# Performance work log

Hardware: AMD Instinct MI355X
Metric: run time of the kernel (lower is better)

Reference implementation:

```python
import jax, jax.numpy as jnp
import numpy as np

EPS = 1e-5

def rmsnorm(x, w):
    var = jnp.mean(x * x, axis=-1, keepdims=True)
    return x * jax.lax.rsqrt(var + EPS) * w

def apply_rope(x, cos, sin):
    # x: [B, S, H, D], cos/sin: [S, D//2]; llama-style complex rotation over pairs
    B, S, H, D = x.shape
    xr = x.reshape(B, S, H, D // 2, 2)
    x0, x1 = xr[..., 0], xr[..., 1]
    c = cos[None, :, None, :]
    s = sin[None, :, None, :]
    o0 = x0 * c - x1 * s
    o1 = x0 * s + x1 * c
    return jnp.stack([o0, o1], axis=-1).reshape(B, S, H, D)

def setup_inputs() -> dict:
    key = jax.random.key(0)
    ks = jax.random.split(key, 8)
    B, S, dim = 2, 2048, 2048
    H, nope, rope = 16, 128, 64
    q_lr, kv_lr = 1536, 512
    hd = nope + rope
    x = jax.random.normal(ks[0], (B, S, dim), jnp.float32)
    wd_q = jax.random.normal(ks[1], (dim, q_lr), jnp.float32) * (dim ** -0.5)
    wu_q = jax.random.normal(ks[2], (q_lr, H * hd), jnp.float32) * (q_lr ** -0.5)
    q_norm_w = jnp.ones((q_lr,), jnp.float32)
    wd_kv = jax.random.normal(ks[3], (dim, kv_lr + rope), jnp.float32) * (dim ** -0.5)
    wu_kv = jax.random.normal(ks[4], (kv_lr, H * 2 * nope), jnp.float32) * (kv_lr ** -0.5)
    kv_norm_w = jnp.ones((kv_lr,), jnp.float32)
    wo = jax.random.normal(ks[5], (H * nope, dim), jnp.float32) * ((H * nope) ** -0.5)
    pos = jnp.arange(S, dtype=jnp.float32)
    inv_freq = 1.0 / (10000.0 ** (jnp.arange(0, rope, 2, dtype=jnp.float32) / rope))
    ang = pos[:, None] * inv_freq[None, :]  # [S, rope//2]
    return {"x": x, "wd_q": wd_q, "wu_q": wu_q, "q_norm_w": q_norm_w,
            "wd_kv": wd_kv, "wu_kv": wu_kv, "kv_norm_w": kv_norm_w, "wo": wo,
            "cos": jnp.cos(ang), "sin": jnp.sin(ang), "start_pos": 0}

def reference(x, wd_q, wu_q, q_norm_w, wd_kv, wu_kv, kv_norm_w, wo, cos, sin, start_pos):
    B, S, dim = x.shape
    H, nope, rope = 16, 128, 64
    kv_lr = 512
    hd = nope + rope
    # low-rank Q projection + RMSNorm
    cq = x @ wd_q
    xq = rmsnorm(cq, q_norm_w) @ wu_q
    xq = xq.reshape(B, S, H, hd)
    xq_nope, xq_rope = xq[..., :nope], xq[..., nope:]
    # low-rank KV projection
    kvd = x @ wd_kv
    ckv, xk_rope = kvd[..., :kv_lr], kvd[..., kv_lr:]
    xk_rope = xk_rope.reshape(B, S, 1, rope)
    kvu = (rmsnorm(ckv, kv_norm_w) @ wu_kv).reshape(B, S, H, 2 * nope)
    xk_nope, xv = kvu[..., :nope], kvu[..., nope:]
    # partial RoPE
    xq_rope = apply_rope(xq_rope, cos, sin)
    xk_rope = apply_rope(xk_rope, cos, sin)
    xk_rope = jnp.broadcast_to(xk_rope, (B, S, H, rope))
    q = jnp.concatenate([xq_nope, xq_rope], axis=-1)  # [B,S,H,192]
    k = jnp.concatenate([xk_nope, xk_rope], axis=-1)
    # causal SDPA
    scale = 1.0 / jnp.sqrt(jnp.float32(hd))
    scores = jnp.einsum('bqhd,bkhd->bhqk', q, k) * scale
    mask = jnp.tril(jnp.ones((S, S), bool))
    scores = jnp.where(mask[None, None], scores, jnp.finfo(scores.dtype).min)
    attn = jax.nn.softmax(scores, axis=-1)
    out = jnp.einsum('bhqk,bkhd->bqhd', attn, xv).reshape(B, S, H * nope)
    return out @ wo
```

## Files before the change

kernel.cpp:

```cpp
#include <hip/hip_runtime.h>
#include <hip/hip_bf16.h>

#define S_LEN 2048
#define NHEAD 16
#define NOPE 128
#define ROPE 64
#define HD 192

typedef unsigned short ushort_t;
typedef __attribute__((ext_vector_type(8))) short short8;
typedef __attribute__((ext_vector_type(4))) float f32x4;

#define AS1 __attribute__((address_space(1)))
#define AS3 __attribute__((address_space(3)))

__device__ __forceinline__ unsigned short f2bf(float f) {
  unsigned int u = __float_as_uint(f);
  return (unsigned short)((u + 0x7FFFu + ((u >> 16) & 1u)) >> 16);
}

__global__ __launch_bounds__(256) void cast_f32_bf16_k(const float* __restrict__ in,
                                                       ushort_t* __restrict__ out) {
  const int i = blockIdx.x * 256 + threadIdx.x;
  const float4 v0 = *(const float4*)&in[(size_t)i * 8];
  const float4 v1 = *(const float4*)&in[(size_t)i * 8 + 4];
  union { uint4 u; ushort_t s[8]; } pk;
  pk.s[0] = f2bf(v0.x); pk.s[1] = f2bf(v0.y); pk.s[2] = f2bf(v0.z); pk.s[3] = f2bf(v0.w);
  pk.s[4] = f2bf(v1.x); pk.s[5] = f2bf(v1.y); pk.s[6] = f2bf(v1.z); pk.s[7] = f2bf(v1.w);
  *(uint4*)&out[(size_t)i * 8] = pk.u;
}

__global__ __launch_bounds__(256) void transpose_cast_k(const float* __restrict__ B,
                                                        ushort_t* __restrict__ Bt,
                                                        int K, int N) {
  __shared__ float tile[32][33];
  const int tx = threadIdx.x & 31, ty = threadIdx.x >> 5;
  const int n0 = blockIdx.x * 32, k0 = blockIdx.y * 32;
  if (n0 >= N) {
#pragma unroll
    for (int r = 0; r < 4; ++r)
      Bt[(size_t)(n0 + ty + 8 * r) * K + k0 + tx] = 0;
    return;
  }
#pragma unroll
  for (int r = 0; r < 4; ++r)
    tile[ty + 8 * r][tx] = B[(size_t)(k0 + ty + 8 * r) * N + n0 + tx];
  __syncthreads();
#pragma unroll
  for (int r = 0; r < 4; ++r)
    Bt[(size_t)(n0 + ty + 8 * r) * K + k0 + tx] = f2bf(tile[tx][ty + 8 * r]);
}

template<int EPI>
__global__ __launch_bounds__(256) void mfma_gemm(const ushort_t* __restrict__ A,
                                                 const ushort_t* __restrict__ Bt,
                                                 float* __restrict__ C,
                                                 int M, int N, int K, int ldc,
                                                 ushort_t* __restrict__ kb16o,
                                                 ushort_t* __restrict__ vto,
                                                 float* __restrict__ C2) {
  __shared__ ushort_t As[128 * 32];
  __shared__ ushort_t Bs[128 * 32];
  const int tid = threadIdx.x;
  const int lane = tid & 63;
  const int wave = tid >> 6;
  const int wm = wave & 1, wn = wave >> 1;

  unsigned bxu = blockIdx.x, byu = blockIdx.y;
  {
    const unsigned gx = gridDim.x;
    const unsigned nwg = gx * gridDim.y;
    if ((nwg & 7u) == 0u) {
      unsigned flat = byu * gx + bxu;
      const unsigned cpx = nwg >> 3;
      flat = (flat & 7u) * cpx + (flat >> 3);
      bxu = flat % gx; byu = flat / gx;
    }
  }
  const int m0 = byu * 128, n0 = bxu * 128;
  const int l15 = lane & 15, quad = lane >> 4;

  f32x4 acc[4][4] = {};

  const int it0 = tid, it1 = tid + 256;
  const int ma0 = it0 >> 2, kc0 = it0 & 3;
  const int ma1 = it1 >> 2, kc1 = it1 & 3;

  typedef AS3 ushort_t lds_us;
  lds_us* AsL = (lds_us*)As;
  lds_us* BsL = (lds_us*)Bs;
  const int wbase = wave * 512;

  for (int k0 = 0; k0 < K; k0 += 32) {
    __builtin_amdgcn_global_load_lds(
        (const AS1 void*)&A[(size_t)(m0 + ma0) * K + k0 + kc0 * 8],
        (AS3 void*)(AsL + wbase), 16, 0, 0);
    __builtin_amdgcn_global_load_lds(
        (const AS1 void*)&A[(size_t)(m0 + ma1) * K + k0 + kc1 * 8],
        (AS3 void*)(AsL + 2048 + wbase), 16, 0, 0);
    __builtin_amdgcn_global_load_lds(
        (const AS1 void*)&Bt[(size_t)(n0 + ma0) * K + k0 + kc0 * 8],
        (AS3 void*)(BsL + wbase), 16, 0, 0);
    __builtin_amdgcn_global_load_lds(
        (const AS1 void*)&Bt[(size_t)(n0 + ma1) * K + k0 + kc1 * 8],
        (AS3 void*)(BsL + 2048 + wbase), 16, 0, 0);
    __syncthreads();

    short8 af[4], bf[4];
#pragma unroll
    for (int i = 0; i < 4; ++i)
      af[i] = *(const short8*)&As[(wm * 64 + i * 16 + l15) * 32 + quad * 8];
#pragma unroll
    for (int j = 0; j < 4; ++j)
      bf[j] = *(const short8*)&Bs[(wn * 64 + j * 16 + l15) * 32 + quad * 8];
#pragma unroll
    for (int i = 0; i < 4; ++i)
#pragma unroll
      for (int j = 0; j < 4; ++j)
        acc[i][j] = __builtin_amdgcn_mfma_f32_16x16x32_bf16(af[i], bf[j], acc[i][j], 0, 0, 0);
    __syncthreads();
  }

  if constexpr (EPI == 0) {
#pragma unroll
    for (int i = 0; i < 4; ++i)
#pragma unroll
      for (int r = 0; r < 4; ++r) {
        const size_t rg = (size_t)(m0 + wm * 64 + i * 16 + quad * 4 + r);
#pragma unroll
        for (int j = 0; j < 4; ++j)
          C[rg * ldc + n0 + wn * 64 + j * 16 + l15] = acc[i][j][r];
      }
  } else if constexpr (EPI == 1) {
    const int h = n0 >> 8;
    const bool is_v = (n0 >> 7) & 1;
    if (!is_v) {
#pragma unroll
      for (int i = 0; i < 4; ++i)
#pragma unroll
        for (int r = 0; r < 4; ++r) {
          const size_t rg = (size_t)(m0 + wm * 64 + i * 16 + quad * 4 + r);
#pragma unroll
          for (int j = 0; j < 4; ++j)
            kb16o[rg * 2048 + h * 128 + wn * 64 + j * 16 + l15] = f2bf(acc[i][j][r]);
        }
    } else {
      __shared__ __align__(16) ushort_t trb[64 * 136];
      const int bb = m0 >> 11;
      const int m0loc = m0 & 2047;
      ushort_t* vbase = vto + ((size_t)(bb * NHEAD + h) * 128) * 2048;
#pragma unroll
      for (int vh = 0; vh < 2; ++vh) {
        if (wn == vh) {
#pragma unroll
          for (int i = 0; i < 4; ++i)
#pragma unroll
            for (int r = 0; r < 4; ++r) {
              const int tloc = wm * 64 + i * 16 + quad * 4 + r;
#pragma unroll
              for (int j = 0; j < 4; ++j)
                trb[(j * 16 + l15) * 136 + tloc] = f2bf(acc[i][j][r]);
            }
        }
        __syncthreads();
#pragma unroll
        for (int it = 0; it < 4; ++it) {
          const int u = tid + (it << 8);
          const int vdl = u >> 4, tc = u & 15;
          *(uint4*)&vbase[(size_t)(vh * 64 + vdl) * 2048 + m0loc + tc * 8] =
              *(const uint4*)&trb[vdl * 136 + tc * 8];
        }
        __syncthreads();
      }
    }
  } else {
    float* Cd;
    int ldd, nc;
    if (n0 < 1536) { Cd = C;  ldd = 1536; nc = n0; }
    else           { Cd = C2; ldd = 640;  nc = n0 - 1536; }
#pragma unroll
    for (int i = 0; i < 4; ++i)
#pragma unroll
      for (int r = 0; r < 4; ++r) {
        const size_t rg = (size_t)(m0 + wm * 64 + i * 16 + quad * 4 + r);
#pragma unroll
        for (int j = 0; j < 4; ++j)
          Cd[rg * ldd + nc + wn * 64 + j * 16 + l15] = acc[i][j][r];
      }
  }
}

__global__ __launch_bounds__(256) void rmsnorm2_k(const float* __restrict__ cq,
                                                  ushort_t* __restrict__ cqn,
                                                  const float* __restrict__ qw,
                                                  const float* __restrict__ kvd,
                                                  ushort_t* __restrict__ ckvn,
                                                  const float* __restrict__ kvw) {
  const bool is_q = blockIdx.x < 4096;
  const int row = blockIdx.x & 4095;
  const int tid = threadIdx.x;
  const float* ip = is_q ? cq + (size_t)row * 1536 : kvd + (size_t)row * 640;
  ushort_t* op = is_q ? cqn + (size_t)row * 1536 : ckvn + (size_t)row * 512;
  const float* w = is_q ? qw : kvw;
  const int L = is_q ? 1536 : 512;
  const int nper = L >> 8;
  float r[6];
  float ss = 0.f;
  for (int j = 0; j < nper; ++j) {
    r[j] = ip[tid + (j << 8)];
    ss += r[j] * r[j];
  }
  for (int off = 32; off; off >>= 1) ss += __shfl_down(ss, off);
  __shared__ float wsum[4];
  __shared__ float scale_s;
  if ((tid & 63) == 0) wsum[tid >> 6] = ss;
  __syncthreads();
  if (tid == 0) {
    float t = wsum[0] + wsum[1] + wsum[2] + wsum[3];
    scale_s = rsqrtf(t / (float)L + 1e-5f);
  }
  __syncthreads();
  const float sc = scale_s;
  for (int j = 0; j < nper; ++j)
    op[tid + (j << 8)] = f2bf(r[j] * sc * w[tid + (j << 8)]);
}

__global__ __launch_bounds__(512) void rope_k(float* __restrict__ qall,
                                              const float* __restrict__ kvd,
                                              ushort_t* __restrict__ krope16,
                                              const float* __restrict__ cosb,
                                              const float* __restrict__ sinb) {
  const int row = blockIdx.x;
  const int s = row & (S_LEN - 1);
  const int tid = threadIdx.x;
  const int d = tid & 31, h = tid >> 5;
  const float c = cosb[s * 32 + d];
  const float sn = sinb[s * 32 + d];
  float* qb = qall + (size_t)row * 3072 + h * HD + NOPE;
  float x0 = qb[2 * d], x1 = qb[2 * d + 1];
  qb[2 * d]     = x0 * c - x1 * sn;
  qb[2 * d + 1] = x0 * sn + x1 * c;
  if (tid < 32) {
    const float* kb = kvd + (size_t)row * 640 + 512;
    float y0 = kb[2 * d], y1 = kb[2 * d + 1];
    union { unsigned int u; ushort_t s2[2]; } pk;
    pk.s2[0] = f2bf(y0 * c - y1 * sn);
    pk.s2[1] = f2bf(y0 * sn + y1 * c);
    *(unsigned int*)&krope16[(size_t)row * 64 + 2 * d] = pk.u;
  }
}

#define QT 128
#define KC 64
__global__ __launch_bounds__(256, 2) void attn_k(const float* __restrict__ qall,
                                                 const ushort_t* __restrict__ kb16,
                                                 const ushort_t* __restrict__ vT,
                                                 const ushort_t* __restrict__ krope16,
                                                 ushort_t* __restrict__ outp) {
  const int bx = blockIdx.x;
  const int second = bx >> 8;
  const int h = (bx >> 4) & 15;
  int tile = bx & 15;
  if (second) tile = 15 - tile;
  const int b = second;
  const int q0 = tile * QT;
  const int tid = threadIdx.x;
  const int lane = tid & 63;
  const int wq = tid >> 6;
  const int l15 = lane & 15, quad = lane >> 4;

  __shared__ __align__(16) ushort_t Kn[64 * 128];
  __shared__ __align__(16) ushort_t Kr[64 * 64];
  __shared__ __align__(16) ushort_t Vt[2][128 * 64];
  __shared__ __align__(16) ushort_t Pb[4][32 * 72];

  const int qbase = q0 + wq * 32;
  const size_t growq = (size_t)b * S_LEN + qbase;
  const ushort_t* vTh = vT + ((size_t)(b * NHEAD + h) * 128) * 2048;
  const size_t bbase = (size_t)b * S_LEN;

  typedef AS3 ushort_t lds_us;
  lds_us* KnL = (lds_us*)Kn;
  lds_us* KrL = (lds_us*)Kr;
  lds_us* VtL = (lds_us*)Vt;
  const int wbase = wq * 512;

  auto issueK = [&](int c) {
    const size_t growk = bbase + (size_t)c * KC;
#pragma unroll
    for (int it = 0; it < 4; ++it) {
      const int u = tid + (it << 8);
      const int key = u >> 4, s = u & 15;
      const int ss = s ^ (key & 7);
      __builtin_amdgcn_global_load_lds(
          (const AS1 void*)&kb16[(growk + key) * 2048 + h * 128 + ss * 8],
          (AS3 void*)(KnL + wbase + it * 2048), 16, 0, 0);
    }
#pragma unroll
    for (int it = 0; it < 2; ++it) {
      const int u = tid + (it << 8);
      const int key = u >> 3, s = u & 7;
      const int ss = s ^ (key & 7);
      __builtin_amdgcn_global_load_lds(
          (const AS1 void*)&krope16[(growk + key) * 64 + ss * 8],
          (AS3 void*)(KrL + wbase + it * 2048), 16, 0, 0);
    }
  };
  auto issueV = [&](int c, int buf) {
    const int j0 = c * KC;
#pragma unroll
    for (int it = 0; it < 4; ++it) {
      const int u = tid + (it << 8);
      const int vd = u >> 3, s = u & 7;
      const int ss = s ^ (vd & 7);
      __builtin_amdgcn_global_load_lds(
          (const AS1 void*)&vTh[(size_t)vd * 2048 + j0 + ss * 8],
          (AS3 void*)(VtL + buf * 8192 + wbase + it * 2048), 16, 0, 0);
    }
  };

  issueK(0);
  issueV(0, 0);
  __builtin_amdgcn_sched_barrier(0);

  const float scale = 0.07216878364870323f;
  short8 qf[2][6];
#pragma unroll
  for (int mt = 0; mt < 2; ++mt)
#pragma unroll
    for (int ks = 0; ks < 6; ++ks) {
      const float* src = &qall[(growq + mt * 16 + l15) * 3072 + h * HD + ks * 32 + quad * 8];
      const float4 v0 = *(const float4*)src;
      const float4 v1 = *(const float4*)(src + 4);
      union { short8 s8; ushort_t u[8]; } pk;
      pk.u[0] = f2bf(v0.x * scale); pk.u[1] = f2bf(v0.y * scale);
      pk.u[2] = f2bf(v0.z * scale); pk.u[3] = f2bf(v0.w * scale);
      pk.u[4] = f2bf(v1.x * scale); pk.u[5] = f2bf(v1.y * scale);
      pk.u[6] = f2bf(v1.z * scale); pk.u[7] = f2bf(v1.w * scale);
      qf[mt][ks] = pk.s8;
    }

  f32x4 oacc[2][8] = {};
  float mrow[2][4], lrow[2][4];
  int q_r[2][4];
#pragma unroll
  for (int mt = 0; mt < 2; ++mt)
#pragma unroll
    for (int r = 0; r < 4; ++r) {
      mrow[mt][r] = -1e30f; lrow[mt][r] = 0.f;
      q_r[mt][r] = qbase + mt * 16 + quad * 4 + r;
    }

  const int nchunk = (q0 + QT) / KC;

  asm volatile("s_waitcnt vmcnt(4)" ::: "memory");
  __builtin_amdgcn_s_barrier();
  __builtin_amdgcn_sched_barrier(0);

  for (int c = 0; c < nchunk; ++c) {
    const int j0 = c * KC;
    const bool more = (c + 1 < nchunk);
    const int buf = c & 1;
    const bool skipw = (j0 > qbase + 31);

    f32x4 sacc[2][4] = {};
    if (!skipw) {
      __builtin_amdgcn_s_setprio(1);
#pragma unroll
      for (int ks = 0; ks < 6; ++ks) {
        short8 kf[4];
        if (ks < 4) {
#pragma unroll
          for (int kt = 0; kt < 4; ++kt)
            kf[kt] = *(const short8*)&Kn[(kt * 16 + l15) * 128 + (((ks * 4 + quad) ^ (l15 & 7)) << 3)];
        } else {
#pragma unroll
          for (int kt = 0; kt < 4; ++kt)
            kf[kt] = *(const short8*)&Kr[(kt * 16 + l15) * 64 + ((((ks - 4) * 4 + quad) ^ (l15 & 7)) << 3)];
        }
#pragma unroll
        for (int mt = 0; mt < 2; ++mt)
#pragma unroll
          for (int kt = 0; kt < 4; ++kt)
            sacc[mt][kt] = __builtin_amdgcn_mfma_f32_16x16x32_bf16(qf[mt][ks], kf[kt], sacc[mt][kt], 0, 0, 0);
      }
      __builtin_amdgcn_s_setprio(0);
    }

    __builtin_amdgcn_s_barrier();
    if (more) issueK(c + 1);
    __builtin_amdgcn_sched_barrier(0);

    if (!skipw) {
      if (j0 + KC - 1 > qbase) {
#pragma unroll
        for (int mt = 0; mt < 2; ++mt)
#pragma unroll
          for (int kt = 0; kt < 4; ++kt) {
            const int key = j0 + kt * 16 + l15;
#pragma unroll
            for (int r = 0; r < 4; ++r)
              sacc[mt][kt][r] = (key <= q_r[mt][r]) ? sacc[mt][kt][r] : -1e30f;
          }
      }
      float pmax[2][4];
#pragma unroll
      for (int mt = 0; mt < 2; ++mt)
#pragma unroll
        for (int r = 0; r < 4; ++r) {
          float mx = fmaxf(fmaxf(sacc[mt][0][r], sacc[mt][1][r]),
                           fmaxf(sacc[mt][2][r], sacc[mt][3][r]));
          mx = fmaxf(mx, __shfl_xor(mx, 1));
          mx = fmaxf(mx, __shfl_xor(mx, 2));
          mx = fmaxf(mx, __shfl_xor(mx, 4));
          mx = fmaxf(mx, __shfl_xor(mx, 8));
          pmax[mt][r] = mx;
        }
      bool need = false;
#pragma unroll
      for (int mt = 0; mt < 2; ++mt)
#pragma unroll
        for (int r = 0; r < 4; ++r)
          need = need || (pmax[mt][r] > mrow[mt][r] + 8.0f);
      const bool upd = __any(need);
      float alpha[2][4];
      if (upd) {
#pragma unroll
        for (int mt = 0; mt < 2; ++mt)
#pragma unroll
          for (int r = 0; r < 4; ++r) {
            const float mn = fmaxf(mrow[mt][r], pmax[mt][r]);
            alpha[mt][r] = __expf(mrow[mt][r] - mn);
            mrow[mt][r] = mn;
          }
      }
#pragma unroll
      for (int mt = 0; mt < 2; ++mt)
#pragma unroll
        for (int kt = 0; kt < 4; ++kt)
#pragma unroll
          for (int r = 0; r < 4; ++r)
            sacc[mt][kt][r] = __expf(sacc[mt][kt][r] - mrow[mt][r]);
#pragma unroll
      for (int mt = 0; mt < 2; ++mt)
#pragma unroll
        for (int r = 0; r < 4; ++r) {
          float rs = sacc[mt][0][r] + sacc[mt][1][r] + sacc[mt][2][r] + sacc[mt][3][r];
          rs += __shfl_xor(rs, 1);
          rs += __shfl_xor(rs, 2);
          rs += __shfl_xor(rs, 4);
          rs += __shfl_xor(rs, 8);
          lrow[mt][r] = upd ? lrow[mt][r] * alpha[mt][r] + rs : lrow[mt][r] + rs;
        }
#pragma unroll
      for (int mt = 0; mt < 2; ++mt)
#pragma unroll
        for (int kt = 0; kt < 4; ++kt)
#pragma unroll
          for (int r = 0; r < 4; ++r)
            Pb[wq][(mt * 16 + quad * 4 + r) * 72 + kt * 16 + l15] = f2bf(sacc[mt][kt][r]);
      if (upd) {
#pragma unroll
        for (int mt = 0; mt < 2; ++mt)
#pragma unroll
          for (int nt = 0; nt < 8; ++nt)
#pragma unroll
            for (int r = 0; r < 4; ++r)
              oacc[mt][nt][r] *= alpha[mt][r];
      }
    }

    if (more) asm volatile("s_waitcnt vmcnt(6)" ::: "memory");
    else      asm volatile("s_waitcnt vmcnt(0)" ::: "memory");
    __builtin_amdgcn_s_barrier();
    __builtin_amdgcn_sched_barrier(0);

    if (!skipw) {
      __builtin_amdgcn_s_setprio(1);
#pragma unroll
      for (int st = 0; st < 2; ++st) {
        short8 pf[2];
#pragma unroll
        for (int mt = 0; mt < 2; ++mt)
          pf[mt] = *(const short8*)&Pb[wq][(mt * 16 + l15) * 72 + st * 32 + quad * 8];
#pragma unroll
        for (int nt = 0; nt < 8; ++nt) {
          const short8 vf = *(const short8*)&Vt[buf][(nt * 16 + l15) * 64 + (((st * 4 + quad) ^ (l15 & 7)) << 3)];
#pragma unroll
          for (int mt = 0; mt < 2; ++mt)
            oacc[mt][nt] = __builtin_amdgcn_mfma_f32_16x16x32_bf16(pf[mt], vf, oacc[mt][nt], 0, 0, 0);
        }
      }
      __builtin_amdgcn_s_setprio(0);
    }

    if (more) {
      issueV(c + 1, buf ^ 1);
      __builtin_amdgcn_sched_barrier(0);
      asm volatile("s_waitcnt vmcnt(4)" ::: "memory");
      __builtin_amdgcn_s_barrier();
      __builtin_amdgcn_sched_barrier(0);
    }
  }

#pragma unroll
  for (int mt = 0; mt < 2; ++mt)
#pragma unroll
    for (int r = 0; r < 4; ++r) {
      const float inv = 1.0f / lrow[mt][r];
      const size_t orow = growq + mt * 16 + quad * 4 + r;
#pragma unroll
      for (int nt = 0; nt < 8; ++nt)
        outp[orow * 2048 + h * 128 + nt * 16 + l15] = f2bf(oacc[mt][nt][r] * inv);
    }
}

extern "C" void kernel_launch(void* const* d_in, const int* in_sizes, int n_in,
                              void* d_out, int out_size, void* d_ws, size_t ws_size,
                              hipStream_t stream) {
  const float* x        = (const float*)d_in[0];
  const float* wd_q     = (const float*)d_in[1];
  const float* wu_q     = (const float*)d_in[2];
  const float* q_norm_w = (const float*)d_in[3];
  const float* wd_kv    = (const float*)d_in[4];
  const float* wu_kv    = (const float*)d_in[5];
  const float* kv_norm_w= (const float*)d_in[6];
  const float* wo       = (const float*)d_in[7];
  const float* cosb     = (const float*)d_in[8];
  const float* sinb     = (const float*)d_in[9];
  float* out = (float*)d_out;

  char* ws = (char*)d_ws;
  float*    qall  = (float*)(ws + 0);
  float*    cq    = (float*)(ws + 0);
  ushort_t* kb16  = (ushort_t*)(ws + 50331648);
  ushort_t* vT    = (ushort_t*)(ws + 67108864);
  ushort_t* xb    = (ushort_t*)(ws + 83886080);
  ushort_t* cqn   = (ushort_t*)(ws + 117440512);
  float*    kvd   = (float*)(ws + 130023424);
  ushort_t* ckvn  = (ushort_t*)(ws + 140509184);
  ushort_t* aoutb = (ushort_t*)(ws + 130023424);
  ushort_t* krope16 = (ushort_t*)(ws + 146800640);
  ushort_t* wdqt  = (ushort_t*)(ws + 147849216);
  ushort_t* wdkvt = (ushort_t*)(ws + 154140672);
  ushort_t* wuqt  = (ushort_t*)(ws + 156762112);
  ushort_t* wukvt = (ushort_t*)(ws + 166199296);
  ushort_t* wot   = (ushort_t*)(ws + 170393600);

  const int M = 2 * S_LEN;
  dim3 blk(256);

  cast_f32_bf16_k<<<4096, blk, 0, stream>>>(x, xb);

  transpose_cast_k<<<dim3(1536 / 32, 2048 / 32), blk, 0, stream>>>(wd_q, wdqt, 2048, 1536);
  transpose_cast_k<<<dim3(640 / 32, 2048 / 32), blk, 0, stream>>>(wd_kv, wdkvt, 2048, 576);
  transpose_cast_k<<<dim3(3072 / 32, 1536 / 32), blk, 0, stream>>>(wu_q, wuqt, 1536, 3072);
  transpose_cast_k<<<dim3(4096 / 32, 512 / 32), blk, 0, stream>>>(wu_kv, wukvt, 512, 4096);
  transpose_cast_k<<<dim3(2048 / 32, 2048 / 32), blk, 0, stream>>>(wo, wot, 2048, 2048);

  mfma_gemm<2><<<dim3(2176 / 128, M / 128), blk, 0, stream>>>(
      xb, wdqt, cq, M, 2176, 2048, 1536, nullptr, nullptr, kvd);
  rmsnorm2_k<<<2 * M, 256, 0, stream>>>(cq, cqn, q_norm_w, kvd, ckvn, kv_norm_w);
  mfma_gemm<0><<<dim3(3072 / 128, M / 128), blk, 0, stream>>>(
      cqn, wuqt, qall, M, 3072, 1536, 3072, nullptr, nullptr, nullptr);
  mfma_gemm<1><<<dim3(4096 / 128, M / 128), blk, 0, stream>>>(
      ckvn, wukvt, nullptr, M, 4096, 512, 0, kb16, vT, nullptr);
  rope_k<<<M, 512, 0, stream>>>(qall, kvd, krope16, cosb, sinb);
  attn_k<<<2 * NHEAD * (S_LEN / QT), 256, 0, stream>>>(qall, kb16, vT, krope16, aoutb);
  mfma_gemm<0><<<dim3(2048 / 128, M / 128), blk, 0, stream>>>(
      aoutb, wot, out, M, 2048, 2048, 2048, nullptr, nullptr, nullptr);
}
```

Baseline: 511.7 us.

## Fuse Q RoPE/scale/bf16 into Q-up GEMM epilogue, merge prep kernels, reorder attention grid

Merges the x cast and five weight transpose-casts into one prep kernel, cutting launch count. The Q up-projection GEMM gets a new epilogue that applies the softmax scale and RoPE (via lane-pair shuffles) and writes bf16 directly. This removes the fp32 Q round trip and the separate Q RoPE pass, and attention now loads bf16 Q fragments directly. The attention block-index mapping is changed to interleave heads and batches with a causal tile pairing for load balance, and the K-rope kernel shrinks to K only.

Result: faster. 496.5 us (-3.0%).

```diff
diff --git a/kernel.cpp b/kernel.cpp
--- a/kernel.cpp
+++ b/kernel.cpp
@@ -19,23 +19,33 @@
   return (unsigned short)((u + 0x7FFFu + ((u >> 16) & 1u)) >> 16);
 }
 
-__global__ __launch_bounds__(256) void cast_f32_bf16_k(const float* __restrict__ in,
-                                                       ushort_t* __restrict__ out) {
-  const int i = blockIdx.x * 256 + threadIdx.x;
-  const float4 v0 = *(const float4*)&in[(size_t)i * 8];
-  const float4 v1 = *(const float4*)&in[(size_t)i * 8 + 4];
-  union { uint4 u; ushort_t s[8]; } pk;
-  pk.s[0] = f2bf(v0.x); pk.s[1] = f2bf(v0.y); pk.s[2] = f2bf(v0.z); pk.s[3] = f2bf(v0.w);
-  pk.s[4] = f2bf(v1.x); pk.s[5] = f2bf(v1.y); pk.s[6] = f2bf(v1.z); pk.s[7] = f2bf(v1.w);
-  *(uint4*)&out[(size_t)i * 8] = pk.u;
-}
-
-__global__ __launch_bounds__(256) void transpose_cast_k(const float* __restrict__ B,
-                                                        ushort_t* __restrict__ Bt,
-                                                        int K, int N) {
+__global__ __launch_bounds__(256) void prep_k(const float* __restrict__ x, ushort_t* __restrict__ xb,
+                                              const float* __restrict__ wd_q, ushort_t* __restrict__ wdqt,
+                                              const float* __restrict__ wd_kv, ushort_t* __restrict__ wdkvt,
+                                              const float* __restrict__ wu_q, ushort_t* __restrict__ wuqt,
+                                              const float* __restrict__ wu_kv, ushort_t* __restrict__ wukvt,
+                                              const float* __restrict__ wo, ushort_t* __restrict__ wot) {
+  int id = blockIdx.x;
+  if (id < 4096) {
+    const int i = id * 256 + threadIdx.x;
+    const float4 v0 = *(const float4*)&x[(size_t)i * 8];
+    const float4 v1 = *(const float4*)&x[(size_t)i * 8 + 4];
+    union { uint4 u; ushort_t s[8]; } pk;
+    pk.s[0] = f2bf(v0.x); pk.s[1] = f2bf(v0.y); pk.s[2] = f2bf(v0.z); pk.s[3] = f2bf(v0.w);
+    pk.s[4] = f2bf(v1.x); pk.s[5] = f2bf(v1.y); pk.s[6] = f2bf(v1.z); pk.s[7] = f2bf(v1.w);
+    *(uint4*)&xb[(size_t)i * 8] = pk.u;
+    return;
+  }
+  id -= 4096;
+  const float* B; ushort_t* Bt; int K, N, gx;
+  if (id < 3072)               { B = wd_q;  Bt = wdqt;  K = 2048; N = 1536; gx = 48;  }
+  else if ((id -= 3072) < 1280){ B = wd_kv; Bt = wdkvt; K = 2048; N = 576;  gx = 20;  }
+  else if ((id -= 1280) < 4608){ B = wu_q;  Bt = wuqt;  K = 1536; N = 3072; gx = 96;  }
+  else if ((id -= 4608) < 2048){ B = wu_kv; Bt = wukvt; K = 512;  N = 4096; gx = 128; }
+  else { id -= 2048;             B = wo;    Bt = wot;   K = 2048; N = 2048; gx = 64;  }
   __shared__ float tile[32][33];
   const int tx = threadIdx.x & 31, ty = threadIdx.x >> 5;
-  const int n0 = blockIdx.x * 32, k0 = blockIdx.y * 32;
+  const int n0 = (id % gx) * 32, k0 = (id / gx) * 32;
   if (n0 >= N) {
 #pragma unroll
     for (int r = 0; r < 4; ++r)
@@ -58,7 +68,9 @@
                                                  int M, int N, int K, int ldc,
                                                  ushort_t* __restrict__ kb16o,
                                                  ushort_t* __restrict__ vto,
-                                                 float* __restrict__ C2) {
+                                                 float* __restrict__ C2,
+                                                 const float* __restrict__ cosb,
+                                                 const float* __restrict__ sinb) {
   __shared__ ushort_t As[128 * 32];
   __shared__ ushort_t Bs[128 * 32];
   const int tid = threadIdx.x;
@@ -173,7 +185,7 @@
         __syncthreads();
       }
     }
-  } else {
+  } else if constexpr (EPI == 2) {
     float* Cd;
     int ldd, nc;
     if (n0 < 1536) { Cd = C;  ldd = 1536; nc = n0; }
@@ -186,6 +198,30 @@
 #pragma unroll
         for (int j = 0; j < 4; ++j)
           Cd[rg * ldd + nc + wn * 64 + j * 16 + l15] = acc[i][j][r];
+      }
+  } else {
+    const float qscale = 0.07216878364870323f;
+#pragma unroll
+    for (int i = 0; i < 4; ++i)
+#pragma unroll
+      for (int r = 0; r < 4; ++r) {
+        const int rg = m0 + wm * 64 + i * 16 + quad * 4 + r;
+        const int sp = rg & (S_LEN - 1);
+#pragma unroll
+        for (int j = 0; j < 4; ++j) {
+          const int col = n0 + wn * 64 + j * 16 + l15;
+          float val = acc[i][j][r] * qscale;
+          const float pr = __shfl_xor(val, 1);
+          const int dd = col % HD;
+          float o = val;
+          if (dd >= NOPE) {
+            const int d = (dd - NOPE) >> 1;
+            const float cc = cosb[sp * 32 + d];
+            const float sn = sinb[sp * 32 + d];
+            o = (lane & 1) ? (pr * sn + val * cc) : (val * cc - pr * sn);
+          }
+          kb16o[(size_t)rg * 3072 + col] = f2bf(o);
+        }
       }
   }
 }
@@ -225,44 +261,36 @@
     op[tid + (j << 8)] = f2bf(r[j] * sc * w[tid + (j << 8)]);
 }
 
-__global__ __launch_bounds__(512) void rope_k(float* __restrict__ qall,
-                                              const float* __restrict__ kvd,
-                                              ushort_t* __restrict__ krope16,
-                                              const float* __restrict__ cosb,
-                                              const float* __restrict__ sinb) {
-  const int row = blockIdx.x;
+__global__ __launch_bounds__(256) void rope_kr_k(const float* __restrict__ kvd,
+                                                 ushort_t* __restrict__ krope16,
+                                                 const float* __restrict__ cosb,
+                                                 const float* __restrict__ sinb) {
+  const int tid = threadIdx.x;
+  const int row = blockIdx.x * 8 + (tid >> 5);
+  const int d = tid & 31;
   const int s = row & (S_LEN - 1);
-  const int tid = threadIdx.x;
-  const int d = tid & 31, h = tid >> 5;
   const float c = cosb[s * 32 + d];
   const float sn = sinb[s * 32 + d];
-  float* qb = qall + (size_t)row * 3072 + h * HD + NOPE;
-  float x0 = qb[2 * d], x1 = qb[2 * d + 1];
-  qb[2 * d]     = x0 * c - x1 * sn;
-  qb[2 * d + 1] = x0 * sn + x1 * c;
-  if (tid < 32) {
-    const float* kb = kvd + (size_t)row * 640 + 512;
-    float y0 = kb[2 * d], y1 = kb[2 * d + 1];
-    union { unsigned int u; ushort_t s2[2]; } pk;
-    pk.s2[0] = f2bf(y0 * c - y1 * sn);
-    pk.s2[1] = f2bf(y0 * sn + y1 * c);
-    *(unsigned int*)&krope16[(size_t)row * 64 + 2 * d] = pk.u;
-  }
+  const float* kb = kvd + (size_t)row * 640 + 512;
+  const float y0 = kb[2 * d], y1 = kb[2 * d + 1];
+  union { unsigned int u; ushort_t s2[2]; } pk;
+  pk.s2[0] = f2bf(y0 * c - y1 * sn);
+  pk.s2[1] = f2bf(y0 * sn + y1 * c);
+  *(unsigned int*)&krope16[(size_t)row * 64 + 2 * d] = pk.u;
 }
 
 #define QT 128
 #define KC 64
-__global__ __launch_bounds__(256, 2) void attn_k(const float* __restrict__ qall,
+__global__ __launch_bounds__(256, 2) void attn_k(const ushort_t* __restrict__ q16,
                                                  const ushort_t* __restrict__ kb16,
                                                  const ushort_t* __restrict__ vT,
                                                  const ushort_t* __restrict__ krope16,
                                                  ushort_t* __restrict__ outp) {
   const int bx = blockIdx.x;
-  const int second = bx >> 8;
-  const int h = (bx >> 4) & 15;
-  int tile = bx & 15;
-  if (second) tile = 15 - tile;
-  const int b = second;
+  const int g = bx & 31;
+  const int s = bx >> 5;
+  const int tile = (s < 8) ? s : 23 - s;
+  const int b = g >> 4, h = g & 15;
   const int q0 = tile * QT;
   const int tid = threadIdx.x;
   const int lane = tid & 63;
@@ -290,8 +318,8 @@
 #pragma unroll
     for (int it = 0; it < 4; ++it) {
       const int u = tid + (it << 8);
-      const int key = u >> 4, s = u & 15;
-      const int ss = s ^ (key & 7);
+      const int key = u >> 4, sl = u & 15;
+      const int ss = sl ^ (key & 7);
       __builtin_amdgcn_global_load_lds(
           (const AS1 void*)&kb16[(growk + key) * 2048 + h * 128 + ss * 8],
           (AS3 void*)(KnL + wbase + it * 2048), 16, 0, 0);
@@ -299,8 +327,8 @@
 #pragma unroll
     for (int it = 0; it < 2; ++it) {
       const int u = tid + (it << 8);
-      const int key = u >> 3, s = u & 7;
-      const int ss = s ^ (key & 7);
+      const int key = u >> 3, sl = u & 7;
+      const int ss = sl ^ (key & 7);
       __builtin_amdgcn_global_load_lds(
           (const AS1 void*)&krope16[(growk + key) * 64 + ss * 8],
           (AS3 void*)(KrL + wbase + it * 2048), 16, 0, 0);
@@ -311,8 +339,8 @@
 #pragma unroll
     for (int it = 0; it < 4; ++it) {
       const int u = tid + (it << 8);
-      const int vd = u >> 3, s = u & 7;
-      const int ss = s ^ (vd & 7);
+      const int vd = u >> 3, sl = u & 7;
+      const int ss = sl ^ (vd & 7);
       __builtin_amdgcn_global_load_lds(
           (const AS1 void*)&vTh[(size_t)vd * 2048 + j0 + ss * 8],
           (AS3 void*)(VtL + buf * 8192 + wbase + it * 2048), 16, 0, 0);
@@ -323,22 +351,12 @@
   issueV(0, 0);
   __builtin_amdgcn_sched_barrier(0);
 
-  const float scale = 0.07216878364870323f;
   short8 qf[2][6];
 #pragma unroll
   for (int mt = 0; mt < 2; ++mt)
 #pragma unroll
-    for (int ks = 0; ks < 6; ++ks) {
-      const float* src = &qall[(growq + mt * 16 + l15) * 3072 + h * HD + ks * 32 + quad * 8];
-      const float4 v0 = *(const float4*)src;
-      const float4 v1 = *(const float4*)(src + 4);
-      union { short8 s8; ushort_t u[8]; } pk;
-      pk.u[0] = f2bf(v0.x * scale); pk.u[1] = f2bf(v0.y * scale);
-      pk.u[2] = f2bf(v0.z * scale); pk.u[3] = f2bf(v0.w * scale);
-      pk.u[4] = f2bf(v1.x * scale); pk.u[5] = f2bf(v1.y * scale);
-      pk.u[6] = f2bf(v1.z * scale); pk.u[7] = f2bf(v1.w * scale);
-      qf[mt][ks] = pk.s8;
-    }
+    for (int ks = 0; ks < 6; ++ks)
+      qf[mt][ks] = *(const short8*)&q16[(growq + mt * 16 + l15) * 3072 + h * HD + ks * 32 + quad * 8];
 
   f32x4 oacc[2][8] = {};
   float mrow[2][4], lrow[2][4];
@@ -531,8 +549,8 @@
   float* out = (float*)d_out;
 
   char* ws = (char*)d_ws;
-  float*    qall  = (float*)(ws + 0);
   float*    cq    = (float*)(ws + 0);
+  ushort_t* q16   = (ushort_t*)(ws + 0);
   ushort_t* kb16  = (ushort_t*)(ws + 50331648);
   ushort_t* vT    = (ushort_t*)(ws + 67108864);
   ushort_t* xb    = (ushort_t*)(ws + 83886080);
@@ -550,23 +568,18 @@
   const int M = 2 * S_LEN;
   dim3 blk(256);
 
-  cast_f32_bf16_k<<<4096, blk, 0, stream>>>(x, xb);
-
-  transpose_cast_k<<<dim3(1536 / 32, 2048 / 32), blk, 0, stream>>>(wd_q, wdqt, 2048, 1536);
-  transpose_cast_k<<<dim3(640 / 32, 2048 / 32), blk, 0, stream>>>(wd_kv, wdkvt, 2048, 576);
-  transpose_cast_k<<<dim3(3072 / 32, 1536 / 32), blk, 0, stream>>>(wu_q, wuqt, 1536, 3072);
-  transpose_cast_k<<<dim3(4096 / 32, 512 / 32), blk, 0, stream>>>(wu_kv, wukvt, 512, 4096);
-  transpose_cast_k<<<dim3(2048 / 32, 2048 / 32), blk, 0, stream>>>(wo, wot, 2048, 2048);
+  prep_k<<<19200, blk, 0, stream>>>(x, xb, wd_q, wdqt, wd_kv, wdkvt,
+                                    wu_q, wuqt, wu_kv, wukvt, wo, wot);
 
   mfma_gemm<2><<<dim3(2176 / 128, M / 128), blk, 0, stream>>>(
-      xb, wdqt, cq, M, 2176, 2048, 1536, nullptr, nullptr, kvd);
+      xb, wdqt, cq, M, 2176, 2048, 1536, nullptr, nullptr, kvd, nullptr, nullptr);
   rmsnorm2_k<<<2 * M, 256, 0, stream>>>(cq, cqn, q_norm_w, kvd, ckvn, kv_norm_w);
-  mfma_gemm<0><<<dim3(3072 / 128, M / 128), blk, 0, stream>>>(
-      cqn, wuqt, qall, M, 3072, 1536, 3072, nullptr, nullptr, nullptr);
+  mfma_gemm<3><<<dim3(3072 / 128, M / 128), blk, 0, stream>>>(
+      cqn, wuqt, nullptr, M, 3072, 1536, 0, q16, nullptr, nullptr, cosb, sinb);
   mfma_gemm<1><<<dim3(4096 / 128, M / 128), blk, 0, stream>>>(
-      ckvn, wukvt, nullptr, M, 4096, 512, 0, kb16, vT, nullptr);
-  rope_k<<<M, 512, 0, stream>>>(qall, kvd, krope16, cosb, sinb);
-  attn_k<<<2 * NHEAD * (S_LEN / QT), 256, 0, stream>>>(qall, kb16, vT, krope16, aoutb);
+      ckvn, wukvt, nullptr, M, 4096, 512, 0, kb16, vT, nullptr, nullptr, nullptr);
+  rope_kr_k<<<512, blk, 0, stream>>>(kvd, krope16, cosb, sinb);
+  attn_k<<<2 * NHEAD * (S_LEN / QT), 256, 0, stream>>>(q16, kb16, vT, krope16, aoutb);
   mfma_gemm<0><<<dim3(2048 / 128, M / 128), blk, 0, stream>>>(
-      aoutb, wot, out, M, 2048, 2048, 2048, nullptr, nullptr, nullptr);
-}
+      aoutb, wot, out, M, 2048, 2048, 2048, nullptr, nullptr, nullptr, nullptr, nullptr);
+}
```
